# Kernel tuning notes

Hardware: AMD Instinct MI355X
Metric: run time of the kernel (lower is better)

The kernel has to match this reference:

```python
import jax, jax.numpy as jnp
import numpy as np

B, H, W, C, WS, NH = 32, 56, 56, 384, 7, 12
HD = C // NH            # head dim = 32
HID = 4 * C             # mlp hidden = 1536
SCALE = HD ** -0.5
EPS = 1e-5


def setup_inputs() -> dict:
    key = jax.random.key(0)
    ks = jax.random.split(key, 12)
    w = lambda k, shape: jax.random.normal(k, shape, jnp.float32) * 0.02
    return {
        "x": jax.random.normal(ks[0], (B, H * W, C), jnp.float32),
        "ln1_w": jnp.ones((C,), jnp.float32),
        "ln1_b": jnp.zeros((C,), jnp.float32),
        "qkv_w": w(ks[1], (3 * C, C)),          # nn.Linear weight [out,in], no bias
        "proj_w": w(ks[2], (C, C)),
        "proj_b": jnp.zeros((C,), jnp.float32),
        "ln2_w": jnp.ones((C,), jnp.float32),
        "ln2_b": jnp.zeros((C,), jnp.float32),
        "fc1_w": w(ks[3], (HID, C)),
        "fc1_b": jnp.zeros((HID,), jnp.float32),
        "fc2_w": w(ks[4], (C, HID)),
        "fc2_b": jnp.zeros((C,), jnp.float32),
    }


def _layer_norm(x, w, b):
    mu = jnp.mean(x, axis=-1, keepdims=True)
    var = jnp.mean((x - mu) ** 2, axis=-1, keepdims=True)
    return (x - mu) * jax.lax.rsqrt(var + EPS) * w + b


def _window_partition(x):
    # x: [B, H, W, C] -> [B*nW, WS*WS, C]
    x = x.reshape(B, H // WS, WS, W // WS, WS, C)
    x = x.transpose(0, 1, 3, 2, 4, 5)
    return x.reshape(-1, WS * WS, C)


def _window_reverse(xw):
    # [B*nW, WS*WS, C] -> [B, H*W, C]
    x = xw.reshape(B, H // WS, W // WS, WS, WS, C)
    x = x.transpose(0, 1, 3, 2, 4, 5)
    return x.reshape(B, H * W, C)


def reference(x, ln1_w, ln1_b, qkv_w, proj_w, proj_b, ln2_w, ln2_b,
              fc1_w, fc1_b, fc2_w, fc2_b):
    h = x
    xn = _layer_norm(x, ln1_w, ln1_b)
    xw = _window_partition(xn.reshape(B, H, W, C))      # [nB, N, C], N = 49

    # windowed multi-head self-attention
    qkv = xw @ qkv_w.T                                  # [nB, N, 3C]
    q, k, v = jnp.split(qkv, 3, axis=-1)
    def heads(t):
        return t.reshape(t.shape[0], t.shape[1], NH, HD).transpose(0, 2, 1, 3)
    q, k, v = heads(q), heads(k), heads(v)              # [nB, NH, N, HD]
    attn = jnp.einsum('bhnd,bhmd->bhnm', q, k) * SCALE
    attn = jax.nn.softmax(attn, axis=-1)
    out = jnp.einsum('bhnm,bhmd->bhnd', attn, v)        # [nB, NH, N, HD]
    out = out.transpose(0, 2, 1, 3).reshape(xw.shape[0], WS * WS, C)
    out = out @ proj_w.T + proj_b

    x = h + _window_reverse(out)

    # MLP (note: GELU applied after both fc1 and fc2, as in source)
    h = x
    xn = _layer_norm(x, ln2_w, ln2_b)
    y = jax.nn.gelu(xn @ fc1_w.T + fc1_b, approximate=False)
    y = jax.nn.gelu(y @ fc2_w.T + fc2_b, approximate=False)
    return h + y
```

## Files before the change

### kernel.cpp

```cpp
#include <hip/hip_runtime.h>
#include <cstdint>

#define TOKENS 100352
#define CDIM 384
#define HIDDIM 1536
#define NQKV 1152
#define NHEAD 12
#define NWIN_ALL 2048

typedef __bf16 bf16x8 __attribute__((ext_vector_type(8)));
typedef float f32x4 __attribute__((ext_vector_type(4)));
typedef unsigned short u16;
typedef u16 u16x8 __attribute__((ext_vector_type(8)));

typedef __attribute__((address_space(1))) unsigned int u32_as1;
typedef __attribute__((address_space(3))) unsigned int u32_as3;

__device__ __forceinline__ float bf2f(u16 u) {
    union { unsigned int i; float f; } v; v.i = ((unsigned int)u) << 16; return v.f;
}
__device__ __forceinline__ u16 f2bf(float f) {
    union { float f; unsigned int i; } v; v.f = f;
    unsigned int i = v.i;
    i += 0x7fffu + ((i >> 16) & 1u);
    return (u16)(i >> 16);
}
__device__ __forceinline__ float gelu_f(float x) {
    const float u = x * (0.7978845608028654f + 0.035677408136300125f * x * x);
    const float a = __builtin_fabsf(u);
    const float e = __expf(2.0f * a);
    float t = 1.0f - 2.0f * __builtin_amdgcn_rcpf(e + 1.0f);
    t = __builtin_copysignf(t, u);
    return 0.5f * x * (1.0f + t);
}
__device__ __forceinline__ void gload16(const u16* g, u16* l) {
    __builtin_amdgcn_global_load_lds((const u32_as1*)g, (u32_as3*)l, 16, 0, 0);
}

__global__ void cvt_kernel(const float* __restrict__ in, u16* __restrict__ out, int n) {
    int i = blockIdx.x * blockDim.x + threadIdx.x;
    if (i < n) out[i] = f2bf(in[i]);
}

__global__ __launch_bounds__(256) void ln_kernel(const float* __restrict__ x,
                                                 const float* __restrict__ w,
                                                 const float* __restrict__ b,
                                                 u16* __restrict__ out) {
    const int wid = threadIdx.x >> 6, lane = threadIdx.x & 63;
    const long row = (long)blockIdx.x * 4 + wid;
    const float* xr = x + row * CDIM;
    float v[6];
#pragma unroll
    for (int i = 0; i < 6; i++) v[i] = xr[lane + i * 64];
    float s = 0.f;
#pragma unroll
    for (int i = 0; i < 6; i++) s += v[i];
#pragma unroll
    for (int off = 32; off >= 1; off >>= 1) s += __shfl_xor(s, off, 64);
    const float mu = s * (1.0f / CDIM);
    float q = 0.f;
#pragma unroll
    for (int i = 0; i < 6; i++) { float d = v[i] - mu; q += d * d; }
#pragma unroll
    for (int off = 32; off >= 1; off >>= 1) q += __shfl_xor(q, off, 64);
    const float rs = rsqrtf(q * (1.0f / CDIM) + 1e-5f);
    u16* orow = out + row * CDIM;
#pragma unroll
    for (int i = 0; i < 6; i++) {
        const int c = lane + i * 64;
        orow[c] = f2bf((v[i] - mu) * rs * w[c] + b[c]);
    }
}

template <int EPI>
__global__ __launch_bounds__(256, 2) void gemm_kernel(const u16* __restrict__ A,
                                                      const u16* __restrict__ Bw,
                                                      const float* __restrict__ bias,
                                                      const float* __restrict__ res,
                                                      void* __restrict__ outp,
                                                      int N, int K) {
    __shared__ u16 lsA0[128 * 64];
    __shared__ u16 lsB0[128 * 64];
    __shared__ u16 lsA1[128 * 64];
    __shared__ u16 lsB1[128 * 64];
    const int ntiles = N >> 7;
    const int nwg = gridDim.x;
    const int bid = blockIdx.x;
    const int wg = ((nwg & 7) == 0) ? ((bid & 7) * (nwg >> 3) + (bid >> 3)) : bid;
    const int tm = wg / ntiles, tn = wg % ntiles;
    const int tid = threadIdx.x, wid = tid >> 6, lane = tid & 63;
    const int wr = wid >> 1, wc = wid & 1;

    const int srow = wid * 32 + (lane >> 3);
    const int schunk = (lane & 7) ^ (lane >> 3);
    const u16* gA = A + (size_t)(tm * 128 + srow) * K + schunk * 8;
    const u16* gB = Bw + (size_t)(tn * 128 + srow) * K + schunk * 8;
    const size_t rskip = (size_t)8 * K;
    const int lofs = wid * 2048;

    f32x4 acc[4][4] = {};

    const int rA = wr * 64 + (lane & 15);
    const int rB = wc * 64 + (lane & 15);
    const int ksub = lane >> 4;
    const int rx = lane & 7;

    auto STAGE = [&](u16* la, u16* lb, int kofs) {
#pragma unroll
        for (int j = 0; j < 4; j++) {
            gload16(gA + kofs + j * rskip, la + lofs + j * 512);
            gload16(gB + kofs + j * rskip, lb + lofs + j * 512);
        }
    };
    auto COMPUTE = [&](const u16* la, const u16* lb) {
#pragma unroll
        for (int kk = 0; kk < 2; kk++) {
            const int ca = (((kk << 2) + ksub) ^ rx) << 3;
            bf16x8 af[4], bfr[4];
#pragma unroll
            for (int mi = 0; mi < 4; mi++)
                af[mi] = *(const bf16x8*)(la + (rA + mi * 16) * 64 + ca);
#pragma unroll
            for (int ni = 0; ni < 4; ni++)
                bfr[ni] = *(const bf16x8*)(lb + (rB + ni * 16) * 64 + ca);
#pragma unroll
            for (int mi = 0; mi < 4; mi++)
#pragma unroll
                for (int ni = 0; ni < 4; ni++)
                    acc[mi][ni] = __builtin_amdgcn_mfma_f32_16x16x32_bf16(af[mi], bfr[ni], acc[mi][ni], 0, 0, 0);
        }
    };

    STAGE(lsA0, lsB0, 0);
    __syncthreads();
    const int nt = K >> 6;
    for (int t = 0; t < nt; t += 2) {
        STAGE(lsA1, lsB1, (t + 1) << 6);
        COMPUTE(lsA0, lsB0);
        __syncthreads();
        if (t + 2 < nt) STAGE(lsA0, lsB0, (t + 2) << 6);
        COMPUTE(lsA1, lsB1);
        __syncthreads();
    }

    const int r0 = tm * 128 + wr * 64 + ((lane >> 4) << 2);
    const int c0 = tn * 128 + wc * 64 + (lane & 15);
#pragma unroll
    for (int ni = 0; ni < 4; ni++) {
        const int col = c0 + ni * 16;
        const float bc = (EPI == 0) ? 0.0f : bias[col];
#pragma unroll
        for (int mi = 0; mi < 4; mi++) {
#pragma unroll
            for (int r = 0; r < 4; r++) {
                const size_t row = (size_t)(r0 + mi * 16 + r);
                const size_t idx = row * (size_t)N + col;
                const float v = acc[mi][ni][r];
                if (EPI == 1)      ((float*)outp)[idx] = v + bc + res[idx];
                else if (EPI == 2) ((u16*)outp)[idx] = f2bf(gelu_f(v + bc));
                else if (EPI == 3) ((float*)outp)[idx] = res[idx] + gelu_f(v + bc);
                else               ((u16*)outp)[idx] = f2bf(v);
            }
        }
    }
}

__global__ __launch_bounds__(256, 4) void attn_kernel(const u16* __restrict__ qkv,
                                                      u16* __restrict__ out) {
    __shared__ u16 pbuf[4 * 64 * 64];
    const int wid = threadIdx.x >> 6, lane = threadIdx.x & 63;
    const int id = blockIdx.x * 4 + wid;
    const int head = id % NHEAD;
    const int win = id / NHEAD;
    const int b = win >> 6, wy = (win >> 3) & 7, wx = win & 7;
    const int base_tok = b * 3136 + wy * 392 + wx * 7;
    const int l15 = lane & 15, lg = lane >> 4;
    u16* pw = pbuf + wid * 4096;

    bf16x8 qf[4], kf[4];
#pragma unroll
    for (int t4 = 0; t4 < 4; t4++) {
        const int r = t4 * 16 + l15;
        if (r < 49) {
            const size_t to = (size_t)(base_tok + (r / 7) * 56 + (r % 7)) * NQKV + head * 32 + lg * 8;
            qf[t4] = *(const bf16x8*)(qkv + to);
            kf[t4] = *(const bf16x8*)(qkv + to + 384);
        } else {
#pragma unroll
            for (int j = 0; j < 8; j++) { qf[t4][j] = (__bf16)0.0f; kf[t4][j] = (__bf16)0.0f; }
        }
    }

    f32x4 s[4][4] = {};
#pragma unroll
    for (int qt = 0; qt < 4; qt++)
#pragma unroll
        for (int nt = 0; nt < 4; nt++)
            s[qt][nt] = __builtin_amdgcn_mfma_f32_16x16x32_bf16(qf[qt], kf[nt], s[qt][nt], 0, 0, 0);

    const float NEG = -1e30f;
    if (l15 >= 1) {
#pragma unroll
        for (int qt = 0; qt < 4; qt++)
#pragma unroll
            for (int r = 0; r < 4; r++) s[qt][3][r] = NEG;
    }
    float rm[4][4], inv[4][4];
#pragma unroll
    for (int qt = 0; qt < 4; qt++)
#pragma unroll
        for (int r = 0; r < 4; r++) {
            float m = fmaxf(fmaxf(s[qt][0][r], s[qt][1][r]), fmaxf(s[qt][2][r], s[qt][3][r]));
#pragma unroll
            for (int off = 1; off <= 8; off <<= 1) m = fmaxf(m, __shfl_xor(m, off, 64));
            rm[qt][r] = m;
        }
    const float cexp = 0.25508682f;
#pragma unroll
    for (int qt = 0; qt < 4; qt++)
#pragma unroll
        for (int nt = 0; nt < 4; nt++)
#pragma unroll
            for (int r = 0; r < 4; r++)
                s[qt][nt][r] = exp2f((s[qt][nt][r] - rm[qt][r]) * cexp);
#pragma unroll
    for (int qt = 0; qt < 4; qt++)
#pragma unroll
        for (int r = 0; r < 4; r++) {
            float su = s[qt][0][r] + s[qt][1][r] + s[qt][2][r] + s[qt][3][r];
#pragma unroll
            for (int off = 1; off <= 8; off <<= 1) su += __shfl_xor(su, off, 64);
            inv[qt][r] = 1.0f / su;
        }

#pragma unroll
    for (int qt = 0; qt < 4; qt++)
#pragma unroll
        for (int nt = 0; nt < 4; nt++)
#pragma unroll
            for (int r = 0; r < 4; r++) {
                const int row = qt * 16 + lg * 4 + r;
                const int col = nt * 16 + l15;
                pw[row * 64 + (((col >> 3) ^ (row & 7)) << 3) + (col & 7)] = f2bf(s[qt][nt][r]);
            }

    u16x8 vtu[2][2];
#pragma unroll
    for (int ks = 0; ks < 2; ks++)
#pragma unroll
        for (int j = 0; j < 8; j++) {
            const int k = ks * 32 + lg * 8 + j;
            u16 v0 = 0, v1 = 0;
            if (k < 49) {
                const size_t to = (size_t)(base_tok + (k / 7) * 56 + (k % 7)) * NQKV + 768 + head * 32 + l15;
                v0 = qkv[to]; v1 = qkv[to + 16];
            }
            vtu[0][ks][j] = v0; vtu[1][ks][j] = v1;
        }

    f32x4 oa[4][2] = {};
#pragma unroll
    for (int ks = 0; ks < 2; ks++) {
        bf16x8 pa[4];
#pragma unroll
        for (int qt = 0; qt < 4; qt++) {
            const int row = qt * 16 + l15;
            pa[qt] = *(const bf16x8*)(pw + row * 64 + (((ks * 4 + lg) ^ (row & 7)) << 3));
        }
#pragma unroll
        for (int qt = 0; qt < 4; qt++)
#pragma unroll
            for (int dt = 0; dt < 2; dt++)
                oa[qt][dt] = __builtin_amdgcn_mfma_f32_16x16x32_bf16(
                    pa[qt], *(const bf16x8*)&vtu[dt][ks], oa[qt][dt], 0, 0, 0);
    }

#pragma unroll
    for (int qt = 0; qt < 4; qt++)
#pragma unroll
        for (int r = 0; r < 4; r++) {
            const int row = qt * 16 + lg * 4 + r;
            if (row < 49) {
                const int t = base_tok + (row / 7) * 56 + (row % 7);
                u16* dst = out + (size_t)t * CDIM + head * 32 + l15;
                dst[0]  = f2bf(oa[qt][0][r] * inv[qt][r]);
                dst[16] = f2bf(oa[qt][1][r] * inv[qt][r]);
            }
        }
}

extern "C" void kernel_launch(void* const* d_in, const int* in_sizes, int n_in,
                              void* d_out, int out_size, void* d_ws, size_t ws_size,
                              hipStream_t stream) {
    const float* x     = (const float*)d_in[0];
    const float* ln1w  = (const float*)d_in[1];
    const float* ln1b  = (const float*)d_in[2];
    const float* qkvw  = (const float*)d_in[3];
    const float* projw = (const float*)d_in[4];
    const float* projb = (const float*)d_in[5];
    const float* ln2w  = (const float*)d_in[6];
    const float* ln2b  = (const float*)d_in[7];
    const float* fc1w  = (const float*)d_in[8];
    const float* fc1b  = (const float*)d_in[9];
    const float* fc2w  = (const float*)d_in[10];
    const float* fc2b  = (const float*)d_in[11];
    float* out = (float*)d_out;

    const size_t sz_xn = (size_t)TOKENS * CDIM * 2;
    const size_t sz_w  = ((size_t)NQKV * CDIM + (size_t)CDIM * CDIM +
                          (size_t)HIDDIM * CDIM + (size_t)CDIM * HIDDIM) * 2;
    if (sz_xn + sz_w > ws_size) return;
    const size_t avail = ws_size - sz_xn - sz_w;

    int nc_a = 1;
    while (nc_a <= 32 && (size_t)(TOKENS / nc_a) * NQKV * 2 > avail) nc_a <<= 1;
    int nc_m = 1;
    while (nc_m <= 16 && (size_t)(TOKENS / nc_m) * HIDDIM * 2 > avail) nc_m <<= 1;
    if (nc_a > 32 || nc_m > 16) return;

    char* ws = (char*)d_ws;
    u16* xn   = (u16*)ws;  ws += sz_xn;
    u16* wq = (u16*)ws; ws += (size_t)NQKV * CDIM * 2;
    u16* wp = (u16*)ws; ws += (size_t)CDIM * CDIM * 2;
    u16* w1 = (u16*)ws; ws += (size_t)HIDDIM * CDIM * 2;
    u16* w2 = (u16*)ws; ws += (size_t)CDIM * HIDDIM * 2;
    u16* cbuf = (u16*)ws;

    cvt_kernel<<<(NQKV * CDIM + 255) / 256, 256, 0, stream>>>(qkvw, wq, NQKV * CDIM);
    cvt_kernel<<<(CDIM * CDIM + 255) / 256, 256, 0, stream>>>(projw, wp, CDIM * CDIM);
    cvt_kernel<<<(HIDDIM * CDIM + 255) / 256, 256, 0, stream>>>(fc1w, w1, HIDDIM * CDIM);
    cvt_kernel<<<(CDIM * HIDDIM + 255) / 256, 256, 0, stream>>>(fc2w, w2, CDIM * HIDDIM);

    ln_kernel<<<TOKENS / 4, 256, 0, stream>>>(x, ln1w, ln1b, xn);

    {
        const int ctok = TOKENS / nc_a;
        const int cwin = NWIN_ALL / nc_a;
        for (int c = 0; c < nc_a; c++) {
            u16* xnc = xn + (size_t)c * ctok * CDIM;
            gemm_kernel<0><<<(ctok / 128) * (NQKV / 128), 256, 0, stream>>>(
                xnc, wq, nullptr, nullptr, cbuf, NQKV, CDIM);
            attn_kernel<<<(cwin * NHEAD) / 4, 256, 0, stream>>>(cbuf, xnc);
        }
    }

    gemm_kernel<1><<<(TOKENS / 128) * (CDIM / 128), 256, 0, stream>>>(
        xn, wp, projb, x, out, CDIM, CDIM);

    ln_kernel<<<TOKENS / 4, 256, 0, stream>>>(out, ln2w, ln2b, xn);

    {
        const int ctok = TOKENS / nc_m;
        for (int c = 0; c < nc_m; c++) {
            const u16* xnc = xn + (size_t)c * ctok * CDIM;
            float* outc = out + (size_t)c * ctok * CDIM;
            gemm_kernel<2><<<(ctok / 128) * (HIDDIM / 128), 256, 0, stream>>>(
                xnc, w1, fc1b, nullptr, cbuf, HIDDIM, CDIM);
            gemm_kernel<3><<<(ctok / 128) * (CDIM / 128), 256, 0, stream>>>(
                cbuf, w2, fc2b, outc, outc, CDIM, HIDDIM);
        }
    }
}
```

Measured before the change: 1.096 ms.

## Load GEMM B fragments directly from global memory, halving LDS use

The GEMM kernel no longer stages the weight (B) tiles through shared memory. Each wave now reads its B fragments straight from global memory into registers, while A keeps its double-buffered LDS path. With half the LDS per block, the launch bound goes from 2 to 4 blocks per CU, aiming for higher occupancy. The cost is that B is loaded redundantly, by both wave rows and across blocks, with uncoalesced 16-byte loads that are not hidden behind the LDS pipeline. Register pressure under the tighter launch bound may also force spills.

```diff
diff --git a/kernel.cpp b/kernel.cpp
--- a/kernel.cpp
+++ b/kernel.cpp
@@ -73,16 +73,14 @@
 }
 
 template <int EPI>
-__global__ __launch_bounds__(256, 2) void gemm_kernel(const u16* __restrict__ A,
+__global__ __launch_bounds__(256, 4) void gemm_kernel(const u16* __restrict__ A,
                                                       const u16* __restrict__ Bw,
                                                       const float* __restrict__ bias,
                                                       const float* __restrict__ res,
                                                       void* __restrict__ outp,
                                                       int N, int K) {
     __shared__ u16 lsA0[128 * 64];
-    __shared__ u16 lsB0[128 * 64];
     __shared__ u16 lsA1[128 * 64];
-    __shared__ u16 lsB1[128 * 64];
     const int ntiles = N >> 7;
     const int nwg = gridDim.x;
     const int bid = blockIdx.x;
@@ -90,61 +88,63 @@
     const int tm = wg / ntiles, tn = wg % ntiles;
     const int tid = threadIdx.x, wid = tid >> 6, lane = tid & 63;
     const int wr = wid >> 1, wc = wid & 1;
+    const int l15 = lane & 15, lg = lane >> 4;
 
     const int srow = wid * 32 + (lane >> 3);
     const int schunk = (lane & 7) ^ (lane >> 3);
     const u16* gA = A + (size_t)(tm * 128 + srow) * K + schunk * 8;
-    const u16* gB = Bw + (size_t)(tn * 128 + srow) * K + schunk * 8;
     const size_t rskip = (size_t)8 * K;
     const int lofs = wid * 2048;
 
+    const u16* gBf = Bw + (size_t)(tn * 128 + wc * 64 + l15) * K + lg * 8;
+
     f32x4 acc[4][4] = {};
 
-    const int rA = wr * 64 + (lane & 15);
-    const int rB = wc * 64 + (lane & 15);
-    const int ksub = lane >> 4;
+    const int rA = wr * 64 + l15;
+    const int ksub = lg;
     const int rx = lane & 7;
 
-    auto STAGE = [&](u16* la, u16* lb, int kofs) {
-#pragma unroll
-        for (int j = 0; j < 4; j++) {
+    auto STAGE = [&](u16* la, int kofs) {
+#pragma unroll
+        for (int j = 0; j < 4; j++)
             gload16(gA + kofs + j * rskip, la + lofs + j * 512);
-            gload16(gB + kofs + j * rskip, lb + lofs + j * 512);
-        }
     };
-    auto COMPUTE = [&](const u16* la, const u16* lb) {
+    auto COMPUTE = [&](const u16* la, int k0) {
+        bf16x8 bfr[2][4];
+#pragma unroll
+        for (int kk = 0; kk < 2; kk++)
+#pragma unroll
+            for (int ni = 0; ni < 4; ni++)
+                bfr[kk][ni] = *(const bf16x8*)(gBf + (size_t)ni * 16 * K + k0 + kk * 32);
 #pragma unroll
         for (int kk = 0; kk < 2; kk++) {
             const int ca = (((kk << 2) + ksub) ^ rx) << 3;
-            bf16x8 af[4], bfr[4];
+            bf16x8 af[4];
 #pragma unroll
             for (int mi = 0; mi < 4; mi++)
                 af[mi] = *(const bf16x8*)(la + (rA + mi * 16) * 64 + ca);
 #pragma unroll
-            for (int ni = 0; ni < 4; ni++)
-                bfr[ni] = *(const bf16x8*)(lb + (rB + ni * 16) * 64 + ca);
-#pragma unroll
             for (int mi = 0; mi < 4; mi++)
 #pragma unroll
                 for (int ni = 0; ni < 4; ni++)
-                    acc[mi][ni] = __builtin_amdgcn_mfma_f32_16x16x32_bf16(af[mi], bfr[ni], acc[mi][ni], 0, 0, 0);
+                    acc[mi][ni] = __builtin_amdgcn_mfma_f32_16x16x32_bf16(af[mi], bfr[kk][ni], acc[mi][ni], 0, 0, 0);
         }
     };
 
-    STAGE(lsA0, lsB0, 0);
+    STAGE(lsA0, 0);
     __syncthreads();
     const int nt = K >> 6;
     for (int t = 0; t < nt; t += 2) {
-        STAGE(lsA1, lsB1, (t + 1) << 6);
-        COMPUTE(lsA0, lsB0);
+        STAGE(lsA1, (t + 1) << 6);
+        COMPUTE(lsA0, t << 6);
         __syncthreads();
-        if (t + 2 < nt) STAGE(lsA0, lsB0, (t + 2) << 6);
-        COMPUTE(lsA1, lsB1);
+        if (t + 2 < nt) STAGE(lsA0, (t + 2) << 6);
+        COMPUTE(lsA1, (t + 1) << 6);
         __syncthreads();
     }
 
-    const int r0 = tm * 128 + wr * 64 + ((lane >> 4) << 2);
-    const int c0 = tn * 128 + wc * 64 + (lane & 15);
+    const int r0 = tm * 128 + wr * 64 + (lg << 2);
+    const int c0 = tn * 128 + wc * 64 + l15;
 #pragma unroll
     for (int ni = 0; ni < 4; ni++) {
         const int col = c0 + ni * 16;
```

Result: slower. 1.637 ms (+49.4%).
